# Kernel optimization log

Measured on AMD Instinct MI355X. Metric: run time of the kernel, lower is better.

## Reference

```python
import jax, jax.numpy as jnp
import numpy as np
import math

B, DIN, H, W = 8, 192, 32, 32
K, DH = 4096, 32

def setup_inputs() -> dict:
    key = jax.random.key(0)
    ks = jax.random.split(key, 8)
    latent = jax.random.normal(ks[0], (B, DIN, H, W), dtype=jnp.float32)
    # kaiming-uniform-ish codebook
    bound = math.sqrt(6.0 / DH)
    codebook = jax.random.uniform(ks[1], (K, DH), minval=-bound, maxval=bound, dtype=jnp.float32)
    wv_w = jax.random.normal(ks[2], (DH, DIN), dtype=jnp.float32) / math.sqrt(DIN)
    wv_b = jax.random.normal(ks[3], (DH,), dtype=jnp.float32) * 0.01
    wq_w = jax.random.normal(ks[4], (DIN, DH), dtype=jnp.float32) / math.sqrt(DH)
    wq_b = jax.random.normal(ks[5], (DIN,), dtype=jnp.float32) * 0.01
    temp1 = jnp.ones((), dtype=jnp.float32)
    u = jax.random.uniform(ks[6], (B, H, W, K), minval=1e-7, maxval=1.0 - 1e-7, dtype=jnp.float32)
    gumbel = -jnp.log(-jnp.log(u))
    return {"latent": latent, "codebook": codebook, "wv_w": wv_w, "wv_b": wv_b,
            "wq_w": wq_w, "wq_b": wq_b, "temp1": temp1, "gumbel": gumbel,
            "temperature": 1}

def _get_logit(x, c):
    x2 = jnp.sum(x * x, axis=-1, keepdims=True)
    c2 = jnp.sum(c * c, axis=-1)
    inter = jnp.einsum('bhwd,kd->bhwk', x, c)
    return -(x2 + c2 - 2.0 * inter)

def reference(latent, codebook, wv_w, wv_b, wq_w, wq_b, temp1, gumbel, temperature):
    q = jnp.transpose(latent, (0, 2, 3, 1))           # [B,H,W,DIN]
    raw = jnp.einsum('bhwi,oi->bhwo', q, wv_w) + wv_b  # [B,H,W,DH]
    logitRaw = _get_logit(raw, codebook)               # [B,H,W,K]
    t = jnp.float32(temperature)
    logit = logitRaw / (temp1 * t)
    trueCode = jnp.argmax(logit, axis=-1)
    tau = jnp.sqrt(t)
    y_soft = jax.nn.softmax((logit + gumbel) / tau, axis=-1)
    y_hard = jax.nn.one_hot(jnp.argmax(y_soft, axis=-1), logit.shape[-1], dtype=y_soft.dtype)
    sample = y_soft + jax.lax.stop_gradient(y_hard - y_soft)  # straight-through
    code = jnp.argmax(sample, axis=-1)
    quantized = jnp.einsum('bhwk,kd->bhwd', sample, codebook)  # [B,H,W,DH]
    hard = jnp.einsum('bhwd,od->bhwo', quantized, wq_w) + wq_b  # [B,H,W,DIN]
    hard = jnp.transpose(hard, (0, 3, 1, 2))                    # [B,DIN,H,W]
    return hard, code, trueCode, logitRaw, raw, quantized, codebook
```

## Files before the change

kernel.cpp:

```cpp
#include <hip/hip_runtime.h>
#include <math.h>

#define NPIX 8192
#define KCB  4096
#define DH   32
#define DIN  192
#define PB   4
#define EPS  2e-3f

__global__ void k_prep(const float* __restrict__ cb, double* __restrict__ c2d,
                       float* __restrict__ c2f, float4* __restrict__ cbT4) {
  int k = blockIdx.x * 256 + threadIdx.x;
  const float4* rp = (const float4*)(cb + k * DH);
  double s = 0.0;
  #pragma unroll
  for (int j = 0; j < DH / 4; ++j) {
    float4 v = rp[j];
    cbT4[j * KCB + k] = v;
    s = fma((double)v.x, (double)v.x, s);
    s = fma((double)v.y, (double)v.y, s);
    s = fma((double)v.z, (double)v.z, s);
    s = fma((double)v.w, (double)v.w, s);
  }
  c2d[k] = s;
  c2f[k] = (float)s;
}

__global__ void k_copy(const float* __restrict__ src, float* __restrict__ dst) {
  int i = blockIdx.x * 256 + threadIdx.x;
  dst[i] = src[i];
}

__global__ __launch_bounds__(256) void k_raw(const float* __restrict__ latent,
    const float* __restrict__ wv_w, const float* __restrict__ wv_b,
    float* __restrict__ raw_out, float* __restrict__ x2_out) {
  __shared__ float wv[DH * 193];
  for (int idx = threadIdx.x; idx < DH * DIN; idx += 256) {
    int o = idx / DIN, i = idx - o * DIN;
    wv[o * 193 + i] = wv_w[idx];
  }
  __syncthreads();
  const int p = blockIdx.x * 8 + (threadIdx.x >> 5);
  const int o = threadIdx.x & 31;
  const int b = p >> 10, hw = p & 1023;
  const float* lp = latent + b * (DIN * 1024) + hw;
  float acc = wv_b[o];
  #pragma unroll 8
  for (int i = 0; i < DIN; ++i) acc = fmaf(lp[i * 1024], wv[o * 193 + i], acc);
  raw_out[p * DH + o] = acc;
  float s = acc * acc;
  #pragma unroll
  for (int m = 16; m; m >>= 1) s += __shfl_xor(s, m, 64);
  if (o == 0) x2_out[p] = s;
}

__device__ inline unsigned long long packkey(float v, int idx) {
  unsigned int u = __float_as_uint(v);
  u = (u & 0x80000000u) ? ~u : (u | 0x80000000u);
  return ((unsigned long long)u << 32) | (unsigned int)(~idx);
}

__device__ inline float rfl(float x) {
  return __uint_as_float(__builtin_amdgcn_readfirstlane(__float_as_uint(x)));
}

__global__ __launch_bounds__(256) void k_main(
    const float* __restrict__ raw_g, const float* __restrict__ x2_g,
    const float4* __restrict__ cbT4, const float* __restrict__ cb,
    const float* __restrict__ c2f, const float* __restrict__ gumbel,
    const float* __restrict__ temp1p, const int* __restrict__ tempp,
    float* __restrict__ logit_out, float* __restrict__ code_out,
    float* __restrict__ true_out, float* __restrict__ quant_out,
    int* __restrict__ flags) {
  __shared__ unsigned long long redk[2][PB][4];
  __shared__ float              redb[2][2][PB][4];
  __shared__ int code_s[PB];

  const int tid  = threadIdx.x;
  const int pix0 = blockIdx.x * PB;

  float sr[2][DH];
  #pragma unroll
  for (int p = 0; p < 2; ++p)
    #pragma unroll
    for (int d = 0; d < DH; ++d)
      sr[p][d] = rfl(raw_g[(pix0 + p) * DH + d]);

  float vr[2][DH];
  #pragma unroll
  for (int p = 0; p < 2; ++p)
    #pragma unroll
    for (int j = 0; j < DH / 4; ++j) {
      float4 t = *(const float4*)&raw_g[(pix0 + 2 + p) * DH + 4 * j];
      asm("" : "+v"(t.x), "+v"(t.y), "+v"(t.z), "+v"(t.w));
      vr[p][4 * j + 0] = t.x; vr[p][4 * j + 1] = t.y;
      vr[p][4 * j + 2] = t.z; vr[p][4 * j + 3] = t.w;
    }

  const float inv_tt = rfl((float)(1.0 / ((double)(*temp1p) * (double)(*tempp))));
  float x2r[PB];
  int   rb[PB];
  #pragma unroll
  for (int p = 0; p < PB; ++p) {
    x2r[p] = rfl(x2_g[pix0 + p]);
    rb[p]  = (pix0 + p) * KCB;
  }

  float bl[PB], bl2[PB], bg[PB], bg2[PB];
  int   bli[PB], bgi[PB];
  #pragma unroll
  for (int p = 0; p < PB; ++p) {
    bl[p] = -INFINITY; bl2[p] = -INFINITY;
    bg[p] = -INFINITY; bg2[p] = -INFINITY;
    bli[p] = 0; bgi[p] = 0;
  }

  float gfc[PB], gfn[PB];
  float c2c, c2n;
  c2c = c2f[tid];
  #pragma unroll
  for (int p = 0; p < PB; ++p) gfc[p] = gumbel[rb[p] + tid];

  #pragma unroll 1
  for (int c = 0; c < 16; ++c) {
    const int k = c * 256 + tid;

    if (c < 15) {
      c2n = c2f[k + 256];
      #pragma unroll
      for (int p = 0; p < PB; ++p) gfn[p] = gumbel[rb[p] + k + 256];
    }

    float4 cv[8];
    #pragma unroll
    for (int j = 0; j < 8; ++j) cv[j] = cbT4[j * KCB + k];

    float dots[PB];
    #pragma unroll
    for (int p = 0; p < PB; ++p) dots[p] = 0.f;
    #pragma unroll
    for (int j = 0; j < 8; ++j) {
      dots[0] = fmaf(cv[j].x, sr[0][4 * j + 0], dots[0]);
      dots[0] = fmaf(cv[j].y, sr[0][4 * j + 1], dots[0]);
      dots[0] = fmaf(cv[j].z, sr[0][4 * j + 2], dots[0]);
      dots[0] = fmaf(cv[j].w, sr[0][4 * j + 3], dots[0]);
      dots[1] = fmaf(cv[j].x, sr[1][4 * j + 0], dots[1]);
      dots[1] = fmaf(cv[j].y, sr[1][4 * j + 1], dots[1]);
      dots[1] = fmaf(cv[j].z, sr[1][4 * j + 2], dots[1]);
      dots[1] = fmaf(cv[j].w, sr[1][4 * j + 3], dots[1]);
      dots[2] = fmaf(cv[j].x, vr[0][4 * j + 0], dots[2]);
      dots[2] = fmaf(cv[j].y, vr[0][4 * j + 1], dots[2]);
      dots[2] = fmaf(cv[j].z, vr[0][4 * j + 2], dots[2]);
      dots[2] = fmaf(cv[j].w, vr[0][4 * j + 3], dots[2]);
      dots[3] = fmaf(cv[j].x, vr[1][4 * j + 0], dots[3]);
      dots[3] = fmaf(cv[j].y, vr[1][4 * j + 1], dots[3]);
      dots[3] = fmaf(cv[j].z, vr[1][4 * j + 2], dots[3]);
      dots[3] = fmaf(cv[j].w, vr[1][4 * j + 3], dots[3]);
    }

    #pragma unroll
    for (int p = 0; p < PB; ++p) {
      float v = fmaf(2.f, dots[p], -(x2r[p] + c2c));
      __builtin_nontemporal_store(v, &logit_out[rb[p] + k]);
      bool bt = v > bl[p];
      bl2[p] = bt ? bl[p] : fmaxf(bl2[p], v);
      bli[p] = bt ? k : bli[p];
      bl[p]  = bt ? v : bl[p];
      float z = fmaf(v, inv_tt, gfc[p]);
      bool gt = z > bg[p];
      bg2[p] = gt ? bg[p] : fmaxf(bg2[p], z);
      bgi[p] = gt ? k : bgi[p];
      bg[p]  = gt ? z : bg[p];
    }

    c2c = c2n;
    #pragma unroll
    for (int p = 0; p < PB; ++p) gfc[p] = gfn[p];
  }

  const int wave = tid >> 6;
  const int lane = tid & 63;
  #pragma unroll
  for (int p = 0; p < PB; ++p) {
    unsigned long long kl = packkey(bl[p], bli[p]);
    unsigned long long kg = packkey(bg[p], bgi[p]);
    float b1l = bl[p], b2l = bl2[p], b1g = bg[p], b2g = bg2[p];
    #pragma unroll
    for (int m = 32; m; m >>= 1) {
      unsigned long long o1 = __shfl_xor(kl, m, 64);
      float ob1 = __shfl_xor(b1l, m, 64), ob2 = __shfl_xor(b2l, m, 64);
      b2l = fmaxf(fmaxf(b2l, ob2), fminf(b1l, ob1));
      b1l = fmaxf(b1l, ob1);
      if (o1 > kl) kl = o1;
      unsigned long long o2 = __shfl_xor(kg, m, 64);
      float og1 = __shfl_xor(b1g, m, 64), og2 = __shfl_xor(b2g, m, 64);
      b2g = fmaxf(fmaxf(b2g, og2), fminf(b1g, og1));
      b1g = fmaxf(b1g, og1);
      if (o2 > kg) kg = o2;
    }
    if (lane == 0) {
      redk[0][p][wave] = kl;  redk[1][p][wave] = kg;
      redb[0][0][p][wave] = b1l; redb[0][1][p][wave] = b2l;
      redb[1][0][p][wave] = b1g; redb[1][1][p][wave] = b2g;
    }
  }
  __syncthreads();
  if (tid < PB) {
    const int p = tid;
    unsigned long long kl = redk[0][p][0], kg = redk[1][p][0];
    float b1l = redb[0][0][p][0], b2l = redb[0][1][p][0];
    float b1g = redb[1][0][p][0], b2g = redb[1][1][p][0];
    #pragma unroll
    for (int w2 = 1; w2 < 4; ++w2) {
      if (redk[0][p][w2] > kl) kl = redk[0][p][w2];
      if (redk[1][p][w2] > kg) kg = redk[1][p][w2];
      b2l = fmaxf(fmaxf(b2l, redb[0][1][p][w2]), fminf(b1l, redb[0][0][p][w2]));
      b1l = fmaxf(b1l, redb[0][0][p][w2]);
      b2g = fmaxf(fmaxf(b2g, redb[1][1][p][w2]), fminf(b1g, redb[1][0][p][w2]));
      b1g = fmaxf(b1g, redb[1][0][p][w2]);
    }
    int ti = (int)(~(unsigned int)kl);
    int ci = (int)(~(unsigned int)kg);
    true_out[pix0 + p] = (float)ti;
    code_out[pix0 + p] = (float)ci;
    code_s[p] = ci;
    flags[pix0 + p] = (b1l - b2l < EPS || b1g - b2g < EPS) ? 1 : 0;
  }
  __syncthreads();
  if (tid < PB * DH)
    quant_out[pix0 * DH + tid] = cb[code_s[tid >> 5] * DH + (tid & 31)];
}

__global__ __launch_bounds__(256) void k_refine(
    const float* __restrict__ latent, const float* __restrict__ wv_w,
    const float* __restrict__ wv_b, const float* __restrict__ cb,
    const double* __restrict__ c2d, const float* __restrict__ gumbel,
    const float* __restrict__ temp1p, const int* __restrict__ tempp,
    float* __restrict__ code_out, float* __restrict__ true_out,
    float* __restrict__ quant_out, const int* __restrict__ flags) {
  const int pix = blockIdx.x;
  if (flags[pix] == 0) return;

  __shared__ double part[DH][8];
  __shared__ double rawd[DH];
  __shared__ double x2sh;
  __shared__ double redv[2][4];
  __shared__ int    redi[2][4];
  __shared__ int    ig_sh;
  const int tid = threadIdx.x;
  const int b = pix >> 10, hw = pix & 1023;

  {
    const int o = tid >> 3, pt = tid & 7;
    const float* lp = latent + b * (DIN * 1024) + hw;
    double acc = 0.0;
    #pragma unroll 4
    for (int i = pt * 24; i < pt * 24 + 24; ++i)
      acc = fma((double)lp[i * 1024], (double)wv_w[o * DIN + i], acc);
    part[o][pt] = acc;
  }
  __syncthreads();
  if (tid < DH) {
    double acc = (double)wv_b[tid];
    #pragma unroll
    for (int j = 0; j < 8; ++j) acc += part[tid][j];
    rawd[tid] = acc;
  }
  __syncthreads();
  if (tid == 0) {
    double s = 0.0;
    #pragma unroll
    for (int d = 0; d < DH; ++d) s = fma(rawd[d], rawd[d], s);
    x2sh = s;
  }
  __syncthreads();

  const double tt  = (double)(*temp1p) * (double)(*tempp);
  const double tau = sqrt((double)(*tempp));
  const double x2  = x2sh;

  double bl = -INFINITY, bg = -INFINITY;
  int il = 0, ig = 0;
  for (int c = 0; c < KCB / 256; ++c) {
    const int k = c * 256 + tid;
    const float4* rp = (const float4*)(cb + k * DH);
    double dot = 0.0;
    #pragma unroll
    for (int j = 0; j < DH / 4; ++j) {
      float4 v = rp[j];
      dot = fma((double)v.x, rawd[4 * j + 0], dot);
      dot = fma((double)v.y, rawd[4 * j + 1], dot);
      dot = fma((double)v.z, rawd[4 * j + 2], dot);
      dot = fma((double)v.w, rawd[4 * j + 3], dot);
    }
    double lraw = -((x2 + c2d[k]) - 2.0 * dot);
    double zt = lraw / tt;
    if (zt > bl) { bl = zt; il = k; }
    double zg = (zt + (double)gumbel[(long long)pix * KCB + k]) / tau;
    if (zg > bg) { bg = zg; ig = k; }
  }

  const int wave = tid >> 6, lane = tid & 63;
  #pragma unroll
  for (int m = 32; m; m >>= 1) {
    double ov = __shfl_xor(bl, m, 64); int oi = __shfl_xor(il, m, 64);
    if (ov > bl || (ov == bl && oi < il)) { bl = ov; il = oi; }
    double og = __shfl_xor(bg, m, 64); int oj = __shfl_xor(ig, m, 64);
    if (og > bg || (og == bg && oj < ig)) { bg = og; ig = oj; }
  }
  if (lane == 0) { redv[0][wave] = bl; redi[0][wave] = il;
                   redv[1][wave] = bg; redi[1][wave] = ig; }
  __syncthreads();
  if (tid == 0) {
    double vl = redv[0][0], vg = redv[1][0];
    int    jl = redi[0][0], jg = redi[1][0];
    for (int w2 = 1; w2 < 4; ++w2) {
      if (redv[0][w2] > vl || (redv[0][w2] == vl && redi[0][w2] < jl)) { vl = redv[0][w2]; jl = redi[0][w2]; }
      if (redv[1][w2] > vg || (redv[1][w2] == vg && redi[1][w2] < jg)) { vg = redv[1][w2]; jg = redi[1][w2]; }
    }
    true_out[pix] = (float)jl;
    code_out[pix] = (float)jg;
    ig_sh = jg;
  }
  __syncthreads();
  if (tid < DH) quant_out[pix * DH + tid] = cb[ig_sh * DH + tid];
}

__global__ __launch_bounds__(256) void k_hard(const float* __restrict__ quant,
    const float* __restrict__ wq_w, const float* __restrict__ wq_b,
    float* __restrict__ hard) {
  __shared__ float wq[DIN * DH];
  __shared__ float qs[32][33];
  const int bh = blockIdx.x;
  const int b = bh >> 5, h = bh & 31;
  for (int idx = threadIdx.x; idx < DIN * DH; idx += 256) wq[idx] = wq_w[idx];
  for (int idx = threadIdx.x; idx < 32 * DH; idx += 256)
    qs[idx >> 5][idx & 31] = quant[bh * (32 * DH) + idx];
  __syncthreads();
  for (int it = 0; it < (DIN * 32) / 256; ++it) {
    const int idx = it * 256 + threadIdx.x;
    const int o = idx >> 5, w = idx & 31;
    float acc = wq_b[o];
    #pragma unroll
    for (int d = 0; d < DH; ++d) acc = fmaf(qs[w][d], wq[o * DH + d], acc);
    hard[((b * DIN + o) * 32 + h) * 32 + w] = acc;
  }
}

extern "C" void kernel_launch(void* const* d_in, const int* in_sizes, int n_in,
                              void* d_out, int out_size, void* d_ws, size_t ws_size,
                              hipStream_t stream) {
  const float* latent      = (const float*)d_in[0];
  const float* cb          = (const float*)d_in[1];
  const float* wv_w        = (const float*)d_in[2];
  const float* wv_b        = (const float*)d_in[3];
  const float* wq_w        = (const float*)d_in[4];
  const float* wq_b        = (const float*)d_in[5];
  const float* temp1       = (const float*)d_in[6];
  const float* gumbel      = (const float*)d_in[7];
  const int*   temperature = (const int*)d_in[8];

  float* out      = (float*)d_out;
  float* hard     = out;
  float* code     = out + 1572864;
  float* true_c   = out + 1581056;
  float* logitRaw = out + 1589248;
  float* raw      = out + 35143680;
  float* quant    = out + 35405824;
  float* cb_out   = out + 35668096;

  char*   ws    = (char*)d_ws;
  double* c2d   = (double*)ws;
  float*  c2f   = (float*)(ws + 32768);
  int*    flags = (int*)(ws + 49152);
  float*  x2f   = (float*)(ws + 81920);
  float4* cbT4  = (float4*)(ws + 131072);

  k_prep<<<KCB / 256, 256, 0, stream>>>(cb, c2d, c2f, cbT4);
  k_copy<<<(KCB * DH) / 256, 256, 0, stream>>>(cb, cb_out);
  k_raw <<<NPIX / 8, 256, 0, stream>>>(latent, wv_w, wv_b, raw, x2f);
  k_main<<<NPIX / PB, 256, 0, stream>>>(raw, x2f, cbT4, cb, c2f, gumbel,
                                        temp1, temperature, logitRaw,
                                        code, true_c, quant, flags);
  k_refine<<<NPIX, 256, 0, stream>>>(latent, wv_w, wv_b, cb, c2d, gumbel,
                                     temp1, temperature, code, true_c, quant, flags);
  k_hard<<<8 * 32, 256, 0, stream>>>(quant, wq_w, wq_b, hard);
}
```

Baseline: 144.6 us.

## Split codebook scan across two blocks per pixel group and merge partial argmaxes

The main distance/softmax-argmax kernel now splits the K=4096 codebook into two halves, launching twice as many blocks that each scan half the codes and write partial top-2 values and indices to workspace. A new merge kernel combines the two halves to produce code, trueCode, the ambiguity flags and the quantized gather. The aim is more parallelism and shorter per-block serial loops, at the cost of redundant raw/x2 loads per half, an extra kernel launch and a workspace round trip.

```diff
diff --git a/kernel.cpp b/kernel.cpp
--- a/kernel.cpp
+++ b/kernel.cpp
@@ -66,18 +66,18 @@
 
 __global__ __launch_bounds__(256) void k_main(
     const float* __restrict__ raw_g, const float* __restrict__ x2_g,
-    const float4* __restrict__ cbT4, const float* __restrict__ cb,
-    const float* __restrict__ c2f, const float* __restrict__ gumbel,
+    const float4* __restrict__ cbT4, const float* __restrict__ c2f,
+    const float* __restrict__ gumbel,
     const float* __restrict__ temp1p, const int* __restrict__ tempp,
-    float* __restrict__ logit_out, float* __restrict__ code_out,
-    float* __restrict__ true_out, float* __restrict__ quant_out,
-    int* __restrict__ flags) {
+    float* __restrict__ logit_out,
+    float4* __restrict__ pl, int2* __restrict__ pi) {
   __shared__ unsigned long long redk[2][PB][4];
   __shared__ float              redb[2][2][PB][4];
-  __shared__ int code_s[PB];
-
-  const int tid  = threadIdx.x;
-  const int pix0 = blockIdx.x * PB;
+
+  const int tid   = threadIdx.x;
+  const int half  = blockIdx.x & 1;
+  const int pix0  = (blockIdx.x >> 1) * PB;
+  const int kbase = half * (KCB / 2);
 
   float sr[2][DH];
   #pragma unroll
@@ -117,15 +117,15 @@
 
   float gfc[PB], gfn[PB];
   float c2c, c2n;
-  c2c = c2f[tid];
-  #pragma unroll
-  for (int p = 0; p < PB; ++p) gfc[p] = gumbel[rb[p] + tid];
+  c2c = c2f[kbase + tid];
+  #pragma unroll
+  for (int p = 0; p < PB; ++p) gfc[p] = gumbel[rb[p] + kbase + tid];
 
   #pragma unroll 1
-  for (int c = 0; c < 16; ++c) {
-    const int k = c * 256 + tid;
-
-    if (c < 15) {
+  for (int c = 0; c < 8; ++c) {
+    const int k = kbase + c * 256 + tid;
+
+    if (c < 7) {
       c2n = c2f[k + 256];
       #pragma unroll
       for (int p = 0; p < PB; ++p) gfn[p] = gumbel[rb[p] + k + 256];
@@ -221,14 +221,39 @@
     }
     int ti = (int)(~(unsigned int)kl);
     int ci = (int)(~(unsigned int)kg);
-    true_out[pix0 + p] = (float)ti;
-    code_out[pix0 + p] = (float)ci;
-    code_s[p] = ci;
-    flags[pix0 + p] = (b1l - b2l < EPS || b1g - b2g < EPS) ? 1 : 0;
-  }
-  __syncthreads();
-  if (tid < PB * DH)
-    quant_out[pix0 * DH + tid] = cb[code_s[tid >> 5] * DH + (tid & 31)];
+    const int idx = (pix0 + p) * 2 + half;
+    pl[idx] = make_float4(b1l, b2l, b1g, b2g);
+    pi[idx] = make_int2(ti, ci);
+  }
+}
+
+__global__ __launch_bounds__(256) void k_merge(
+    const float4* __restrict__ pl, const int2* __restrict__ pi,
+    const float* __restrict__ cb,
+    float* __restrict__ code_out, float* __restrict__ true_out,
+    float* __restrict__ quant_out, int* __restrict__ flags) {
+  __shared__ int code_s[8];
+  const int tid  = threadIdx.x;
+  const int grp  = tid >> 5, lane = tid & 31;
+  const int pix  = blockIdx.x * 8 + grp;
+  if (lane == 0) {
+    float4 a = pl[pix * 2 + 0];
+    float4 b = pl[pix * 2 + 1];
+    int2  ia = pi[pix * 2 + 0];
+    int2  ib = pi[pix * 2 + 1];
+    float b2l = fmaxf(fmaxf(a.y, b.y), fminf(a.x, b.x));
+    float b1l = a.x; int il = ia.x;
+    if (b.x > b1l) { b1l = b.x; il = ib.x; }
+    float b2g = fmaxf(fmaxf(a.w, b.w), fminf(a.z, b.z));
+    float b1g = a.z; int ig = ia.y;
+    if (b.z > b1g) { b1g = b.z; ig = ib.y; }
+    true_out[pix] = (float)il;
+    code_out[pix] = (float)ig;
+    flags[pix] = (b1l - b2l < EPS || b1g - b2g < EPS) ? 1 : 0;
+    code_s[grp] = ig;
+  }
+  __syncthreads();
+  quant_out[pix * DH + lane] = cb[code_s[grp] * DH + lane];
 }
 
 __global__ __launch_bounds__(256) void k_refine(
@@ -375,13 +400,15 @@
   int*    flags = (int*)(ws + 49152);
   float*  x2f   = (float*)(ws + 81920);
   float4* cbT4  = (float4*)(ws + 131072);
+  float4* pl    = (float4*)(ws + 655360);
+  int2*   pi    = (int2*)  (ws + 917504);
 
   k_prep<<<KCB / 256, 256, 0, stream>>>(cb, c2d, c2f, cbT4);
   k_copy<<<(KCB * DH) / 256, 256, 0, stream>>>(cb, cb_out);
   k_raw <<<NPIX / 8, 256, 0, stream>>>(latent, wv_w, wv_b, raw, x2f);
-  k_main<<<NPIX / PB, 256, 0, stream>>>(raw, x2f, cbT4, cb, c2f, gumbel,
-                                        temp1, temperature, logitRaw,
-                                        code, true_c, quant, flags);
+  k_main<<<(NPIX / PB) * 2, 256, 0, stream>>>(raw, x2f, cbT4, c2f, gumbel,
+                                              temp1, temperature, logitRaw, pl, pi);
+  k_merge<<<NPIX / 8, 256, 0, stream>>>(pl, pi, cb, code, true_c, quant, flags);
   k_refine<<<NPIX, 256, 0, stream>>>(latent, wv_w, wv_b, cb, c2d, gumbel,
                                      temp1, temperature, code, true_c, quant, flags);
   k_hard<<<8 * 32, 256, 0, stream>>>(quant, wq_w, wq_b, hard);
```

Measured after the change: 156.7 us. 8.4% more time.
